# Optimization experiments

Hardware: AMD Instinct MI355X
Metric: run time of the kernel (lower is better)

## Reference

```python
import jax, jax.numpy as jnp
import numpy as np

D_MODEL = 1024
NUM_HEADS = 16
DEPTH = D_MODEL // NUM_HEADS
MAX_SEQ = 2048
B, S = 2, 2048


def setup_inputs() -> dict:
    key = jax.random.key(0)
    ks = jax.random.split(key, 12)
    scale = 1.0 / np.sqrt(D_MODEL)
    inp = {
        'q': jax.random.normal(ks[0], (B, S, D_MODEL), jnp.float32),
        'k': jax.random.normal(ks[1], (B, S, D_MODEL), jnp.float32),
        'v': jax.random.normal(ks[2], (B, S, D_MODEL), jnp.float32),
        'mask': jnp.zeros((B, 1, S, S), jnp.float32),
        'wq_w': jax.random.normal(ks[3], (D_MODEL, D_MODEL), jnp.float32) * scale,
        'wq_b': jnp.zeros((D_MODEL,), jnp.float32),
        'wk_w': jax.random.normal(ks[4], (D_MODEL, D_MODEL), jnp.float32) * scale,
        'wk_b': jnp.zeros((D_MODEL,), jnp.float32),
        'wv_w': jax.random.normal(ks[5], (D_MODEL, D_MODEL), jnp.float32) * scale,
        'wv_b': jnp.zeros((D_MODEL,), jnp.float32),
        'dense_w': jax.random.normal(ks[6], (D_MODEL, D_MODEL), jnp.float32) * scale,
        'dense_b': jnp.zeros((D_MODEL,), jnp.float32),
        'rel_bias': jax.random.normal(ks[7], (2 * MAX_SEQ - 1, NUM_HEADS), jnp.float32),
    }
    return inp


def _split_heads(x):
    # [B, S, D_MODEL] -> [B, H, S, depth]
    b, s, _ = x.shape
    return x.reshape(b, s, NUM_HEADS, DEPTH).transpose(0, 2, 1, 3)


def reference(q, k, v, mask, wq_w, wq_b, wk_w, wk_b, wv_w, wv_b, dense_w, dense_b, rel_bias):
    b, s, _ = q.shape
    # torch Linear: y = x @ W.T + b
    qh = _split_heads(q @ wq_w.T + wq_b)
    kh = _split_heads(k @ wk_w.T + wk_b)
    vh = _split_heads(v @ wv_w.T + wv_b)
    logits = jnp.einsum('bhqd,bhkd->bhqk', qh, kh) / jnp.sqrt(jnp.float32(DEPTH))
    # relative position bias gather
    pos = jnp.arange(s)
    idx = jnp.clip(pos[:, None] - pos[None, :] + MAX_SEQ - 1, 0, 2 * MAX_SEQ - 2)  # [S, S]
    pos_bias = rel_bias[idx]                      # [S, S, H]
    pos_bias = pos_bias.transpose(2, 0, 1)[None]  # [1, H, S, S]
    logits = logits + pos_bias + mask * (-1e9)
    attn = jax.nn.softmax(logits, axis=-1)        # dropout is identity in eval
    out = jnp.einsum('bhqk,bhkd->bhqd', attn, vh)
    out = out.transpose(0, 2, 1, 3).reshape(b, s, D_MODEL)
    out = out @ dense_w.T + dense_b
    return out, attn
```

## Files before the change

kernel.cpp:

```cpp
#include <hip/hip_runtime.h>

typedef _Float16 f16x8 __attribute__((ext_vector_type(8)));
typedef _Float16 f16x4 __attribute__((ext_vector_type(4)));
typedef float f32x4 __attribute__((ext_vector_type(4)));
typedef unsigned short u16x8 __attribute__((ext_vector_type(8)));
typedef unsigned int u32;

#define MFMA16H(a, b, c) __builtin_amdgcn_mfma_f32_16x16x32_f16(a, b, c, 0, 0, 0)

#if __has_builtin(__builtin_amdgcn_exp2f)
#define EXP2F(x) __builtin_amdgcn_exp2f(x)
#else
#define EXP2F(x) exp2f(x)
#endif

#define LOG2E 1.44269504088896340736f
#define SHIFT2 5.0f

__device__ __forceinline__ unsigned short f2bf(float x) {
  unsigned u = __float_as_uint(x);
  u += 0x7FFF + ((u >> 16) & 1);
  return (unsigned short)(u >> 16);
}
__device__ __forceinline__ float bf2f(unsigned short h) {
  return __uint_as_float(((unsigned)h) << 16);
}
__device__ __forceinline__ f16x8 ldh8(const _Float16* p) {
  return *reinterpret_cast<const f16x8*>(p);
}
__device__ __forceinline__ u16x8 ldu8(const unsigned short* p) {
  return *reinterpret_cast<const u16x8*>(p);
}
__device__ __forceinline__ f16x8 cvt8(float4 a, float4 b) {
  f16x8 r;
  r[0] = (_Float16)a.x; r[1] = (_Float16)a.y; r[2] = (_Float16)a.z; r[3] = (_Float16)a.w;
  r[4] = (_Float16)b.x; r[5] = (_Float16)b.y; r[6] = (_Float16)b.z; r[7] = (_Float16)b.w;
  return r;
}

__global__ __launch_bounds__(256) void prep_mask_perm(const float* __restrict__ src,
                                                      unsigned short* __restrict__ dst) {
  const int blk = blockIdx.x;
  const int kt = blk & 31, bq = blk >> 5;
  const int b = bq >> 5, qt = bq & 31;
  const int lane = threadIdx.x;
  const int w = lane >> 6, lg = (lane >> 4) & 3, lr = lane & 15;
  const int q0 = qt * 64;
  const float cs = -1e9f * LOG2E;
  unsigned short vals[16];
#pragma unroll
  for (int c = 0; c < 4; ++c)
#pragma unroll
    for (int r = 0; r < 4; ++r) {
      const int qr = q0 + w * 16 + lg * 4 + r;
      const int kc = kt * 64 + c * 16 + lr;
      vals[c * 4 + r] = f2bf(src[((size_t)b * 2048 + qr) * 2048 + kc] * cs);
    }
  uint4* out = reinterpret_cast<uint4*>(dst) + ((size_t)blk * 256 + lane) * 2;
  out[0] = *reinterpret_cast<uint4*>(&vals[0]);
  out[1] = *reinterpret_cast<uint4*>(&vals[8]);
}

__global__ __launch_bounds__(256, 3) void proj_gemm_kernel(
    const float* __restrict__ qin, const float* __restrict__ kin, const float* __restrict__ vin,
    const float* __restrict__ wq, const float* __restrict__ wk, const float* __restrict__ wv,
    const float* __restrict__ bq, const float* __restrict__ bk, const float* __restrict__ bv,
    _Float16* __restrict__ qhf, _Float16* __restrict__ khf, _Float16* __restrict__ vhT) {
  __shared__ __align__(16) _Float16 As[128 * 32];
  __shared__ __align__(16) _Float16 Bs[128 * 32];

  const int mode = blockIdx.x >> 8;
  const int t = blockIdx.x & 255;
  const float* A = mode == 0 ? qin : (mode == 1 ? kin : vin);
  const float* B = mode == 0 ? wq : (mode == 1 ? wk : wv);
  const float* bias = mode == 0 ? bq : (mode == 1 ? bk : bv);
  _Float16* outp = mode == 0 ? qhf : (mode == 1 ? khf : vhT);

  const int tid = threadIdx.x;
  const int tm = t & 31, tn = t >> 5;
  const int m0 = tm * 128, n0 = tn * 128;
  const int w = tid >> 6, l = tid & 63, lg = l >> 4, lr = l & 15;
  const int wr = w >> 1, wc = w & 1;
  const int srow = tid >> 2, scol = (tid & 3) * 8;

  f32x4 acc[4][4] = {};

  for (int kt = 0; kt < 32; ++kt) {
    const int k0 = kt * 32;
    float4 ra[2][2], rb[2][2];
#pragma unroll
    for (int it = 0; it < 2; ++it) {
      const int row = it * 64 + srow;
      const float* pa = A + (size_t)(m0 + row) * 1024 + k0 + scol;
      const float* pb = B + (size_t)(n0 + row) * 1024 + k0 + scol;
      ra[it][0] = *reinterpret_cast<const float4*>(pa);
      ra[it][1] = *reinterpret_cast<const float4*>(pa + 4);
      rb[it][0] = *reinterpret_cast<const float4*>(pb);
      rb[it][1] = *reinterpret_cast<const float4*>(pb + 4);
    }
    __syncthreads();
#pragma unroll
    for (int it = 0; it < 2; ++it) {
      const int eo = (it * 256 + tid) * 8;
      *reinterpret_cast<f16x8*>(As + eo) = cvt8(ra[it][0], ra[it][1]);
      *reinterpret_cast<f16x8*>(Bs + eo) = cvt8(rb[it][0], rb[it][1]);
    }
    __syncthreads();

    f16x8 fa[4], fb[4];
#pragma unroll
    for (int i = 0; i < 4; ++i) {
      fa[i] = ldh8(As + (wr * 64 + i * 16 + lr) * 32 + lg * 8);
      fb[i] = ldh8(Bs + (wc * 64 + i * 16 + lr) * 32 + lg * 8);
    }
#pragma unroll
    for (int i = 0; i < 4; ++i)
#pragma unroll
      for (int j = 0; j < 4; ++j)
        acc[i][j] = MFMA16H(fa[i], fb[j], acc[i][j]);
  }

#pragma unroll
  for (int i = 0; i < 4; ++i) {
    const int mrow = m0 + wr * 64 + i * 16 + lg * 4;
#pragma unroll
    for (int j = 0; j < 4; ++j) {
      const int ncol = n0 + wc * 64 + j * 16 + lr;
      const float bv = bias[ncol];
#pragma unroll
      for (int r = 0; r < 4; ++r) {
        const int m = mrow + r;
        const float v = acc[i][j][r] + bv;
        const int bb = m >> 11, s = m & 2047, hh = ncol >> 6, d = ncol & 63;
        if (mode != 2)
          outp[((size_t)(bb * 16 + hh) * 2048 + s) * 64 + d] = (_Float16)v;
        else
          outp[((size_t)(bb * 16 + hh) * 64 + d) * 2048 + s] = (_Float16)v;
      }
    }
  }
}

__global__ __launch_bounds__(256) void dense_gemm_kernel(
    const _Float16* __restrict__ A, const float* __restrict__ B,
    const float* __restrict__ bias, float* __restrict__ out_f) {
  __shared__ __align__(16) _Float16 As[128 * 32];
  __shared__ __align__(16) _Float16 Bs[128 * 32];

  const int tid = threadIdx.x;
  const int tm = blockIdx.x & 31, tn = blockIdx.x >> 5;
  const int m0 = tm * 128, n0 = tn * 128;
  const int w = tid >> 6, l = tid & 63, lg = l >> 4, lr = l & 15;
  const int wr = w >> 1, wc = w & 1;
  const int srow = tid >> 2, scol = (tid & 3) * 8;

  f32x4 acc[4][4] = {};

  for (int kt = 0; kt < 32; ++kt) {
    const int k0 = kt * 32;
    uint4 ra[2];
    float4 rb[2][2];
#pragma unroll
    for (int it = 0; it < 2; ++it) {
      const int row = it * 64 + srow;
      ra[it] = *reinterpret_cast<const uint4*>(A + (size_t)(m0 + row) * 1024 + k0 + scol);
      const float* pb = B + (size_t)(n0 + row) * 1024 + k0 + scol;
      rb[it][0] = *reinterpret_cast<const float4*>(pb);
      rb[it][1] = *reinterpret_cast<const float4*>(pb + 4);
    }
    __syncthreads();
#pragma unroll
    for (int it = 0; it < 2; ++it) {
      const int eo = (it * 256 + tid) * 8;
      *reinterpret_cast<uint4*>(As + eo) = ra[it];
      *reinterpret_cast<f16x8*>(Bs + eo) = cvt8(rb[it][0], rb[it][1]);
    }
    __syncthreads();

    f16x8 fa[4], fb[4];
#pragma unroll
    for (int i = 0; i < 4; ++i) {
      fa[i] = ldh8(As + (wr * 64 + i * 16 + lr) * 32 + lg * 8);
      fb[i] = ldh8(Bs + (wc * 64 + i * 16 + lr) * 32 + lg * 8);
    }
#pragma unroll
    for (int i = 0; i < 4; ++i)
#pragma unroll
      for (int j = 0; j < 4; ++j)
        acc[i][j] = MFMA16H(fa[i], fb[j], acc[i][j]);
  }

#pragma unroll
  for (int i = 0; i < 4; ++i) {
    const int mrow = m0 + wr * 64 + i * 16 + lg * 4;
#pragma unroll
    for (int j = 0; j < 4; ++j) {
      const int ncol = n0 + wc * 64 + j * 16 + lr;
      const float bv = bias[ncol];
#pragma unroll
      for (int r = 0; r < 4; ++r)
        out_f[(size_t)(mrow + r) * 1024 + ncol] = acc[i][j][r] + bv;
    }
  }
}

__global__ __launch_bounds__(256, 2) void attn_pv_kernel(
    const _Float16* __restrict__ qh, const _Float16* __restrict__ kh,
    const _Float16* __restrict__ vT,
    const float* __restrict__ rel_bias, const unsigned short* __restrict__ mperm,
    _Float16* __restrict__ o_h, _Float16* __restrict__ p16,
    float* __restrict__ scal) {
  __shared__ float rb2[2112];
  __shared__ __align__(16) _Float16 p_lds[64 * 76];

  const int bid = blockIdx.x;
  const int wg = ((bid & 7) << 7) | (bid >> 3);
  const int bh = wg >> 5, qt = wg & 31;
  const int b = bh >> 4, h = bh & 15;
  const int q0 = qt * 64;
  const int tid = threadIdx.x;
  const int w = tid >> 6, l = tid & 63, lg = l >> 4, lr = l & 15;

  for (int t = tid; t < 2111; t += 256)
    rb2[t] = rel_bias[(q0 + t) * 16 + h] * LOG2E - SHIFT2;

  const size_t bh_off = (size_t)bh * 2048 * 64;
  const _Float16* qhb = qh + bh_off;
  const _Float16* khb = kh + bh_off;
  const _Float16* vTb = vT + bh_off;
  const unsigned short* mpb =
      mperm + (((size_t)(b * 32 + qt) * 32) * 256 + tid) * 16;
  _Float16* pbh = p16 + (size_t)bh * 2048 * 2048;

  f16x8 qf[2];
  {
    const size_t qrow = (size_t)(q0 + w * 16 + lr) * 64;
    qf[0] = ldh8(qhb + qrow + lg * 8);
    qf[1] = ldh8(qhb + qrow + 32 + lg * 8);
  }
  __syncthreads();

  const int qbase = w * 16 + lg * 4;
  const float c1 = 0.125f * LOG2E;
  float sacc[4] = {0.f, 0.f, 0.f, 0.f};
  f32x4 acc_o[4] = {};

  f16x8 kA[8], kB[8];
  u16x8 mA[2], mB[2];

  auto loadK = [&](int kt, f16x8* kd, u16x8* md) {
    md[0] = ldu8(mpb + (size_t)kt * 4096);
    md[1] = ldu8(mpb + (size_t)kt * 4096 + 8);
#pragma unroll
    for (int c = 0; c < 4; ++c) {
      const _Float16* kr = khb + (size_t)(kt * 64 + c * 16 + lr) * 64 + lg * 8;
      kd[c * 2] = ldh8(kr);
      kd[c * 2 + 1] = ldh8(kr + 32);
    }
  };

  auto step = [&](int kt, const f16x8* kd, const u16x8* md) {
#pragma unroll
    for (int c = 0; c < 4; ++c) {
      f32x4 acc = {};
      acc = MFMA16H(qf[0], kd[c * 2], acc);
      acc = MFMA16H(qf[1], kd[c * 2 + 1], acc);
      const int kc = kt * 64 + c * 16 + lr;
#pragma unroll
      for (int r = 0; r < 4; ++r) {
        const float mbf = bf2f((unsigned short)md[c >> 1][(c & 1) * 4 + r]);
        const float l2 = fmaf(acc[r], c1, rb2[qbase + r - kc + 2047]) + mbf;
        const float p = EXP2F(l2);
        sacc[r] += p;
        p_lds[(qbase + r) * 76 + c * 16 + lr] = (_Float16)p;
      }
    }
    f16x8 pf0 = ldh8(p_lds + (w * 16 + lr) * 76 + lg * 8);
    f16x8 pf1 = ldh8(p_lds + (w * 16 + lr) * 76 + 32 + lg * 8);
    _Float16* prow = pbh + (size_t)(q0 + w * 16 + lr) * 2048 + kt * 64 + lg * 8;
    *reinterpret_cast<f16x8*>(prow) = pf0;
    *reinterpret_cast<f16x8*>(prow + 32) = pf1;
#pragma unroll
    for (int n = 0; n < 4; ++n) {
      const _Float16* vr = vTb + (size_t)(n * 16 + lr) * 2048 + kt * 64 + lg * 8;
      acc_o[n] = MFMA16H(pf0, ldh8(vr), acc_o[n]);
      acc_o[n] = MFMA16H(pf1, ldh8(vr + 32), acc_o[n]);
    }
  };

  loadK(0, kA, mA);
  for (int kt = 0; kt < 32; kt += 2) {
    loadK(kt + 1, kB, mB);
    step(kt, kA, mA);
    loadK((kt + 2) & 31, kA, mA);
    step(kt + 1, kB, mB);
  }

  float inv_s[4];
#pragma unroll
  for (int r = 0; r < 4; ++r) {
    float s = sacc[r];
    s += __shfl_xor(s, 1);
    s += __shfl_xor(s, 2);
    s += __shfl_xor(s, 4);
    s += __shfl_xor(s, 8);
    inv_s[r] = 1.0f / s;
    if (lr == 0) scal[(size_t)bh * 2048 + q0 + qbase + r] = inv_s[r];
  }

#pragma unroll
  for (int n = 0; n < 4; ++n)
#pragma unroll
    for (int r = 0; r < 4; ++r) {
      const int qr = q0 + qbase + r;
      const int d = n * 16 + lr;
      o_h[((size_t)(b * 2048 + qr) * 16 + h) * 64 + d] = (_Float16)(acc_o[n][r] * inv_s[r]);
    }
}

__global__ __launch_bounds__(256) void fixup_kernel(const _Float16* __restrict__ p16,
                                                    const float* __restrict__ scal,
                                                    float* __restrict__ attn) {
  const long long n8 = 16777216LL;
  const long long stride = (long long)gridDim.x * 256;
  for (long long i = (long long)blockIdx.x * 256 + threadIdx.x; i < n8; i += stride) {
    f16x8 p = reinterpret_cast<const f16x8*>(p16)[i];
    const float s = scal[i >> 8];
    float4 lo = make_float4((float)p[0] * s, (float)p[1] * s,
                            (float)p[2] * s, (float)p[3] * s);
    float4 hi = make_float4((float)p[4] * s, (float)p[5] * s,
                            (float)p[6] * s, (float)p[7] * s);
    reinterpret_cast<float4*>(attn)[2 * i] = lo;
    reinterpret_cast<float4*>(attn)[2 * i + 1] = hi;
  }
}

extern "C" void kernel_launch(void* const* d_in, const int* in_sizes, int n_in,
                              void* d_out, int out_size, void* d_ws, size_t ws_size,
                              hipStream_t stream) {
  const float* q = (const float*)d_in[0];
  const float* k = (const float*)d_in[1];
  const float* v = (const float*)d_in[2];
  const float* mask = (const float*)d_in[3];
  const float* wq_w = (const float*)d_in[4];
  const float* wq_b = (const float*)d_in[5];
  const float* wk_w = (const float*)d_in[6];
  const float* wk_b = (const float*)d_in[7];
  const float* wv_w = (const float*)d_in[8];
  const float* wv_b = (const float*)d_in[9];
  const float* dw = (const float*)d_in[10];
  const float* db = (const float*)d_in[11];
  const float* rel = (const float*)d_in[12];

  char* ws = (char*)d_ws;
  _Float16* qhf  = (_Float16*)(ws + 0);
  _Float16* khf  = (_Float16*)(ws + 8388608);
  _Float16* vhT  = (_Float16*)(ws + 16777216);
  _Float16* o_h  = (_Float16*)(ws + 25165824);
  float* scal    = (float*)(ws + 33554432);
  unsigned short* mperm = (unsigned short*)(ws + 33816576);
  _Float16* p16  = (_Float16*)(ws + 50593792);

  float* out = (float*)d_out;
  float* attn_out = out + 4194304;

  prep_mask_perm<<<2048, 256, 0, stream>>>(mask, mperm);

  proj_gemm_kernel<<<768, 256, 0, stream>>>(q, k, v, wq_w, wk_w, wv_w,
                                            wq_b, wk_b, wv_b, qhf, khf, vhT);

  attn_pv_kernel<<<1024, 256, 0, stream>>>(qhf, khf, vhT, rel, mperm, o_h, p16, scal);

  fixup_kernel<<<4096, 256, 0, stream>>>(p16, scal, attn_out);

  dense_gemm_kernel<<<256, 256, 0, stream>>>(o_h, dw, db, out);
}
```

Before: 611.8 us.

## Pre-convert inputs to fp16, merge kernels, and use nontemporal attn stores

A new prep kernel fuses the mask permutation with an fp32-to-fp16 conversion of q/k/v and all weight matrices, so the projection and dense GEMMs load fp16 directly instead of converting while staging. The dense GEMM and the attention fixup are merged into a single tail kernel launch, and the fixup writes attn with nontemporal stores. The attention kernel drops its double-buffered K/mask prefetch in favour of a simple loop and raises the occupancy hint to 4 blocks. The changes save launches and GEMM conversion work, but add an extra round trip of fp16 activations through memory and lose the explicit load prefetch in attention.

```diff
diff --git a/kernel.cpp b/kernel.cpp
--- a/kernel.cpp
+++ b/kernel.cpp
@@ -31,51 +31,61 @@
 __device__ __forceinline__ u16x8 ldu8(const unsigned short* p) {
   return *reinterpret_cast<const u16x8*>(p);
 }
-__device__ __forceinline__ f16x8 cvt8(float4 a, float4 b) {
-  f16x8 r;
-  r[0] = (_Float16)a.x; r[1] = (_Float16)a.y; r[2] = (_Float16)a.z; r[3] = (_Float16)a.w;
-  r[4] = (_Float16)b.x; r[5] = (_Float16)b.y; r[6] = (_Float16)b.z; r[7] = (_Float16)b.w;
-  return r;
-}
-
-__global__ __launch_bounds__(256) void prep_mask_perm(const float* __restrict__ src,
-                                                      unsigned short* __restrict__ dst) {
-  const int blk = blockIdx.x;
-  const int kt = blk & 31, bq = blk >> 5;
-  const int b = bq >> 5, qt = bq & 31;
-  const int lane = threadIdx.x;
-  const int w = lane >> 6, lg = (lane >> 4) & 3, lr = lane & 15;
-  const int q0 = qt * 64;
-  const float cs = -1e9f * LOG2E;
-  unsigned short vals[16];
-#pragma unroll
-  for (int c = 0; c < 4; ++c)
-#pragma unroll
-    for (int r = 0; r < 4; ++r) {
-      const int qr = q0 + w * 16 + lg * 4 + r;
-      const int kc = kt * 64 + c * 16 + lr;
-      vals[c * 4 + r] = f2bf(src[((size_t)b * 2048 + qr) * 2048 + kc] * cs);
-    }
-  uint4* out = reinterpret_cast<uint4*>(dst) + ((size_t)blk * 256 + lane) * 2;
-  out[0] = *reinterpret_cast<uint4*>(&vals[0]);
-  out[1] = *reinterpret_cast<uint4*>(&vals[8]);
-}
-
-__global__ __launch_bounds__(256, 3) void proj_gemm_kernel(
-    const float* __restrict__ qin, const float* __restrict__ kin, const float* __restrict__ vin,
+
+__global__ __launch_bounds__(256) void prep_kernel(
+    const float* __restrict__ q, const float* __restrict__ k, const float* __restrict__ v,
     const float* __restrict__ wq, const float* __restrict__ wk, const float* __restrict__ wv,
-    const float* __restrict__ bq, const float* __restrict__ bk, const float* __restrict__ bv,
-    _Float16* __restrict__ qhf, _Float16* __restrict__ khf, _Float16* __restrict__ vhT) {
-  __shared__ __align__(16) _Float16 As[128 * 32];
-  __shared__ __align__(16) _Float16 Bs[128 * 32];
-
-  const int mode = blockIdx.x >> 8;
-  const int t = blockIdx.x & 255;
-  const float* A = mode == 0 ? qin : (mode == 1 ? kin : vin);
-  const float* B = mode == 0 ? wq : (mode == 1 ? wk : wv);
-  const float* bias = mode == 0 ? bq : (mode == 1 ? bk : bv);
-  _Float16* outp = mode == 0 ? qhf : (mode == 1 ? khf : vhT);
-
+    const float* __restrict__ dwt, const float* __restrict__ mask,
+    _Float16* __restrict__ qf, _Float16* __restrict__ kf, _Float16* __restrict__ vf,
+    _Float16* __restrict__ wqf, _Float16* __restrict__ wkf, _Float16* __restrict__ wvf,
+    _Float16* __restrict__ dwf, unsigned short* __restrict__ mperm) {
+  if (blockIdx.x < 2048) {
+    const int blk = blockIdx.x;
+    const int kt = blk & 31, bq = blk >> 5;
+    const int b = bq >> 5, qt = bq & 31;
+    const int lane = threadIdx.x;
+    const int w = lane >> 6, lg = (lane >> 4) & 3, lr = lane & 15;
+    const int q0 = qt * 64;
+    const float cs = -1e9f * LOG2E;
+    unsigned short vals[16];
+#pragma unroll
+    for (int c = 0; c < 4; ++c)
+#pragma unroll
+      for (int r = 0; r < 4; ++r) {
+        const int qr = q0 + w * 16 + lg * 4 + r;
+        const int kc = kt * 64 + c * 16 + lr;
+        vals[c * 4 + r] = f2bf(mask[((size_t)b * 2048 + qr) * 2048 + kc] * cs);
+      }
+    uint4* out = reinterpret_cast<uint4*>(mperm) + ((size_t)blk * 256 + lane) * 2;
+    out[0] = *reinterpret_cast<uint4*>(&vals[0]);
+    out[1] = *reinterpret_cast<uint4*>(&vals[8]);
+    return;
+  }
+  const int i = (blockIdx.x - 2048) * 256 + threadIdx.x;
+  const int r = i >> 18;
+  const int j = i & 262143;
+  const float* src;
+  _Float16* dst;
+  int off = 0;
+  if (r < 4)       { src = q;   dst = qf;  off = r * 262144; }
+  else if (r < 8)  { src = k;   dst = kf;  off = (r - 4) * 262144; }
+  else if (r < 12) { src = v;   dst = vf;  off = (r - 8) * 262144; }
+  else if (r == 12){ src = wq;  dst = wqf; }
+  else if (r == 13){ src = wk;  dst = wkf; }
+  else if (r == 14){ src = wv;  dst = wvf; }
+  else             { src = dwt; dst = dwf; }
+  const int g = off + j;
+  float4 x = reinterpret_cast<const float4*>(src)[g];
+  f16x4 h;
+  h[0] = (_Float16)x.x; h[1] = (_Float16)x.y;
+  h[2] = (_Float16)x.z; h[3] = (_Float16)x.w;
+  reinterpret_cast<f16x4*>(dst)[g] = h;
+}
+
+__device__ __forceinline__ void gemm_body(
+    int t, int mode, const _Float16* __restrict__ A, const _Float16* __restrict__ B,
+    const float* __restrict__ bias, _Float16* __restrict__ out_h, float* __restrict__ out_f,
+    _Float16* As, _Float16* Bs) {
   const int tid = threadIdx.x;
   const int tm = t & 31, tn = t >> 5;
   const int m0 = tm * 128, n0 = tn * 128;
@@ -87,23 +97,19 @@
 
   for (int kt = 0; kt < 32; ++kt) {
     const int k0 = kt * 32;
-    float4 ra[2][2], rb[2][2];
+    uint4 ra[2], rb[2];
 #pragma unroll
     for (int it = 0; it < 2; ++it) {
       const int row = it * 64 + srow;
-      const float* pa = A + (size_t)(m0 + row) * 1024 + k0 + scol;
-      const float* pb = B + (size_t)(n0 + row) * 1024 + k0 + scol;
-      ra[it][0] = *reinterpret_cast<const float4*>(pa);
-      ra[it][1] = *reinterpret_cast<const float4*>(pa + 4);
-      rb[it][0] = *reinterpret_cast<const float4*>(pb);
-      rb[it][1] = *reinterpret_cast<const float4*>(pb + 4);
+      ra[it] = *reinterpret_cast<const uint4*>(A + (size_t)(m0 + row) * 1024 + k0 + scol);
+      rb[it] = *reinterpret_cast<const uint4*>(B + (size_t)(n0 + row) * 1024 + k0 + scol);
     }
     __syncthreads();
 #pragma unroll
     for (int it = 0; it < 2; ++it) {
       const int eo = (it * 256 + tid) * 8;
-      *reinterpret_cast<f16x8*>(As + eo) = cvt8(ra[it][0], ra[it][1]);
-      *reinterpret_cast<f16x8*>(Bs + eo) = cvt8(rb[it][0], rb[it][1]);
+      *reinterpret_cast<uint4*>(As + eo) = ra[it];
+      *reinterpret_cast<uint4*>(Bs + eo) = rb[it];
     }
     __syncthreads();
 
@@ -131,80 +137,35 @@
       for (int r = 0; r < 4; ++r) {
         const int m = mrow + r;
         const float v = acc[i][j][r] + bv;
-        const int bb = m >> 11, s = m & 2047, hh = ncol >> 6, d = ncol & 63;
-        if (mode != 2)
-          outp[((size_t)(bb * 16 + hh) * 2048 + s) * 64 + d] = (_Float16)v;
-        else
-          outp[((size_t)(bb * 16 + hh) * 64 + d) * 2048 + s] = (_Float16)v;
+        if (mode == 2) {
+          out_f[(size_t)m * 1024 + ncol] = v;
+        } else {
+          const int bb = m >> 11, s = m & 2047, hh = ncol >> 6, d = ncol & 63;
+          if (mode == 0)
+            out_h[((size_t)(bb * 16 + hh) * 2048 + s) * 64 + d] = (_Float16)v;
+          else
+            out_h[((size_t)(bb * 16 + hh) * 64 + d) * 2048 + s] = (_Float16)v;
+        }
       }
     }
   }
 }
 
-__global__ __launch_bounds__(256) void dense_gemm_kernel(
-    const _Float16* __restrict__ A, const float* __restrict__ B,
-    const float* __restrict__ bias, float* __restrict__ out_f) {
+__global__ __launch_bounds__(256, 3) void proj_gemm_kernel(
+    const _Float16* __restrict__ qf, const _Float16* __restrict__ kf, const _Float16* __restrict__ vf,
+    const _Float16* __restrict__ wqf, const _Float16* __restrict__ wkf, const _Float16* __restrict__ wvf,
+    const float* __restrict__ bq, const float* __restrict__ bk, const float* __restrict__ bv,
+    _Float16* __restrict__ qhf, _Float16* __restrict__ khf, _Float16* __restrict__ vhT) {
   __shared__ __align__(16) _Float16 As[128 * 32];
   __shared__ __align__(16) _Float16 Bs[128 * 32];
-
-  const int tid = threadIdx.x;
-  const int tm = blockIdx.x & 31, tn = blockIdx.x >> 5;
-  const int m0 = tm * 128, n0 = tn * 128;
-  const int w = tid >> 6, l = tid & 63, lg = l >> 4, lr = l & 15;
-  const int wr = w >> 1, wc = w & 1;
-  const int srow = tid >> 2, scol = (tid & 3) * 8;
-
-  f32x4 acc[4][4] = {};
-
-  for (int kt = 0; kt < 32; ++kt) {
-    const int k0 = kt * 32;
-    uint4 ra[2];
-    float4 rb[2][2];
-#pragma unroll
-    for (int it = 0; it < 2; ++it) {
-      const int row = it * 64 + srow;
-      ra[it] = *reinterpret_cast<const uint4*>(A + (size_t)(m0 + row) * 1024 + k0 + scol);
-      const float* pb = B + (size_t)(n0 + row) * 1024 + k0 + scol;
-      rb[it][0] = *reinterpret_cast<const float4*>(pb);
-      rb[it][1] = *reinterpret_cast<const float4*>(pb + 4);
-    }
-    __syncthreads();
-#pragma unroll
-    for (int it = 0; it < 2; ++it) {
-      const int eo = (it * 256 + tid) * 8;
-      *reinterpret_cast<uint4*>(As + eo) = ra[it];
-      *reinterpret_cast<f16x8*>(Bs + eo) = cvt8(rb[it][0], rb[it][1]);
-    }
-    __syncthreads();
-
-    f16x8 fa[4], fb[4];
-#pragma unroll
-    for (int i = 0; i < 4; ++i) {
-      fa[i] = ldh8(As + (wr * 64 + i * 16 + lr) * 32 + lg * 8);
-      fb[i] = ldh8(Bs + (wc * 64 + i * 16 + lr) * 32 + lg * 8);
-    }
-#pragma unroll
-    for (int i = 0; i < 4; ++i)
-#pragma unroll
-      for (int j = 0; j < 4; ++j)
-        acc[i][j] = MFMA16H(fa[i], fb[j], acc[i][j]);
-  }
-
-#pragma unroll
-  for (int i = 0; i < 4; ++i) {
-    const int mrow = m0 + wr * 64 + i * 16 + lg * 4;
-#pragma unroll
-    for (int j = 0; j < 4; ++j) {
-      const int ncol = n0 + wc * 64 + j * 16 + lr;
-      const float bv = bias[ncol];
-#pragma unroll
-      for (int r = 0; r < 4; ++r)
-        out_f[(size_t)(mrow + r) * 1024 + ncol] = acc[i][j][r] + bv;
-    }
-  }
-}
-
-__global__ __launch_bounds__(256, 2) void attn_pv_kernel(
+  const int mode = blockIdx.x >> 8;
+  const int t = blockIdx.x & 255;
+  if (mode == 0)      gemm_body(t, 0, qf, wqf, bq, qhf, nullptr, As, Bs);
+  else if (mode == 1) gemm_body(t, 0, kf, wkf, bk, khf, nullptr, As, Bs);
+  else                gemm_body(t, 1, vf, wvf, bv, vhT, nullptr, As, Bs);
+}
+
+__global__ __launch_bounds__(256, 4) void attn_pv_kernel(
     const _Float16* __restrict__ qh, const _Float16* __restrict__ kh,
     const _Float16* __restrict__ vT,
     const float* __restrict__ rel_bias, const unsigned short* __restrict__ mperm,
@@ -245,30 +206,20 @@
   float sacc[4] = {0.f, 0.f, 0.f, 0.f};
   f32x4 acc_o[4] = {};
 
-  f16x8 kA[8], kB[8];
-  u16x8 mA[2], mB[2];
-
-  auto loadK = [&](int kt, f16x8* kd, u16x8* md) {
-    md[0] = ldu8(mpb + (size_t)kt * 4096);
-    md[1] = ldu8(mpb + (size_t)kt * 4096 + 8);
+  for (int kt = 0; kt < 32; ++kt) {
+    u16x8 m0v = ldu8(mpb + (size_t)kt * 4096);
+    u16x8 m1v = ldu8(mpb + (size_t)kt * 4096 + 8);
 #pragma unroll
     for (int c = 0; c < 4; ++c) {
-      const _Float16* kr = khb + (size_t)(kt * 64 + c * 16 + lr) * 64 + lg * 8;
-      kd[c * 2] = ldh8(kr);
-      kd[c * 2 + 1] = ldh8(kr + 32);
-    }
-  };
-
-  auto step = [&](int kt, const f16x8* kd, const u16x8* md) {
-#pragma unroll
-    for (int c = 0; c < 4; ++c) {
+      const int kc = kt * 64 + c * 16 + lr;
+      const _Float16* kr = khb + (size_t)kc * 64 + lg * 8;
       f32x4 acc = {};
-      acc = MFMA16H(qf[0], kd[c * 2], acc);
-      acc = MFMA16H(qf[1], kd[c * 2 + 1], acc);
-      const int kc = kt * 64 + c * 16 + lr;
+      acc = MFMA16H(qf[0], ldh8(kr), acc);
+      acc = MFMA16H(qf[1], ldh8(kr + 32), acc);
 #pragma unroll
       for (int r = 0; r < 4; ++r) {
-        const float mbf = bf2f((unsigned short)md[c >> 1][(c & 1) * 4 + r]);
+        const float mbf = bf2f((c < 2) ? (unsigned short)m0v[(c & 1) * 4 + r]
+                                       : (unsigned short)m1v[(c & 1) * 4 + r]);
         const float l2 = fmaf(acc[r], c1, rb2[qbase + r - kc + 2047]) + mbf;
         const float p = EXP2F(l2);
         sacc[r] += p;
@@ -286,14 +237,6 @@
       acc_o[n] = MFMA16H(pf0, ldh8(vr), acc_o[n]);
       acc_o[n] = MFMA16H(pf1, ldh8(vr + 32), acc_o[n]);
     }
-  };
-
-  loadK(0, kA, mA);
-  for (int kt = 0; kt < 32; kt += 2) {
-    loadK(kt + 1, kB, mB);
-    step(kt, kA, mA);
-    loadK((kt + 2) & 31, kA, mA);
-    step(kt + 1, kB, mB);
   }
 
   float inv_s[4];
@@ -318,20 +261,30 @@
     }
 }
 
-__global__ __launch_bounds__(256) void fixup_kernel(const _Float16* __restrict__ p16,
-                                                    const float* __restrict__ scal,
-                                                    float* __restrict__ attn) {
+__global__ __launch_bounds__(256) void tail_kernel(
+    const _Float16* __restrict__ A, const _Float16* __restrict__ Bw,
+    const float* __restrict__ bias, float* __restrict__ out_f,
+    const _Float16* __restrict__ p16, const float* __restrict__ scal,
+    float* __restrict__ attn) {
+  __shared__ __align__(16) _Float16 As[128 * 32];
+  __shared__ __align__(16) _Float16 Bs[128 * 32];
+  if (blockIdx.x < 256) {
+    gemm_body(blockIdx.x, 2, A, Bw, bias, nullptr, out_f, As, Bs);
+    return;
+  }
+  f32x4* attnv = reinterpret_cast<f32x4*>(attn);
   const long long n8 = 16777216LL;
-  const long long stride = (long long)gridDim.x * 256;
-  for (long long i = (long long)blockIdx.x * 256 + threadIdx.x; i < n8; i += stride) {
+  const long long stride = (long long)(gridDim.x - 256) * 256;
+  for (long long i = (long long)(blockIdx.x - 256) * 256 + threadIdx.x; i < n8; i += stride) {
     f16x8 p = reinterpret_cast<const f16x8*>(p16)[i];
     const float s = scal[i >> 8];
-    float4 lo = make_float4((float)p[0] * s, (float)p[1] * s,
-                            (float)p[2] * s, (float)p[3] * s);
-    float4 hi = make_float4((float)p[4] * s, (float)p[5] * s,
-                            (float)p[6] * s, (float)p[7] * s);
-    reinterpret_cast<float4*>(attn)[2 * i] = lo;
-    reinterpret_cast<float4*>(attn)[2 * i + 1] = hi;
+    f32x4 lo, hi;
+    lo[0] = (float)p[0] * s; lo[1] = (float)p[1] * s;
+    lo[2] = (float)p[2] * s; lo[3] = (float)p[3] * s;
+    hi[0] = (float)p[4] * s; hi[1] = (float)p[5] * s;
+    hi[2] = (float)p[6] * s; hi[3] = (float)p[7] * s;
+    __builtin_nontemporal_store(lo, attnv + 2 * i);
+    __builtin_nontemporal_store(hi, attnv + 2 * i + 1);
   }
 }
 
@@ -353,25 +306,31 @@
   const float* rel = (const float*)d_in[12];
 
   char* ws = (char*)d_ws;
-  _Float16* qhf  = (_Float16*)(ws + 0);
-  _Float16* khf  = (_Float16*)(ws + 8388608);
-  _Float16* vhT  = (_Float16*)(ws + 16777216);
-  _Float16* o_h  = (_Float16*)(ws + 25165824);
-  float* scal    = (float*)(ws + 33554432);
-  unsigned short* mperm = (unsigned short*)(ws + 33816576);
-  _Float16* p16  = (_Float16*)(ws + 50593792);
+  _Float16* qf_in = (_Float16*)(ws + 0);
+  _Float16* kf_in = (_Float16*)(ws + 8388608);
+  _Float16* vf_in = (_Float16*)(ws + 16777216);
+  _Float16* wqf   = (_Float16*)(ws + 25165824);
+  _Float16* wkf   = (_Float16*)(ws + 27262976);
+  _Float16* wvf   = (_Float16*)(ws + 29360128);
+  _Float16* dwf   = (_Float16*)(ws + 31457280);
+  _Float16* qhf   = (_Float16*)(ws + 33554432);
+  _Float16* khf   = (_Float16*)(ws + 41943040);
+  _Float16* vhT   = (_Float16*)(ws + 50331648);
+  _Float16* o_h   = (_Float16*)(ws + 58720256);
+  float* scal     = (float*)(ws + 67108864);
+  unsigned short* mperm = (unsigned short*)(ws + 67371008);
+  _Float16* p16   = (_Float16*)(ws + 84148224);
 
   float* out = (float*)d_out;
   float* attn_out = out + 4194304;
 
-  prep_mask_perm<<<2048, 256, 0, stream>>>(mask, mperm);
-
-  proj_gemm_kernel<<<768, 256, 0, stream>>>(q, k, v, wq_w, wk_w, wv_w,
+  prep_kernel<<<18432, 256, 0, stream>>>(q, k, v, wq_w, wk_w, wv_w, dw, mask,
+                                         qf_in, kf_in, vf_in, wqf, wkf, wvf, dwf, mperm);
+
+  proj_gemm_kernel<<<768, 256, 0, stream>>>(qf_in, kf_in, vf_in, wqf, wkf, wvf,
                                             wq_b, wk_b, wv_b, qhf, khf, vhT);
 
   attn_pv_kernel<<<1024, 256, 0, stream>>>(qhf, khf, vhT, rel, mperm, o_h, p16, scal);
 
-  fixup_kernel<<<4096, 256, 0, stream>>>(p16, scal, attn_out);
-
-  dense_gemm_kernel<<<256, 256, 0, stream>>>(o_h, dw, db, out);
-}
+  tail_kernel<<<2304, 256, 0, stream>>>(o_h, dwf, db, out, p16, scal, attn_out);
+}
```

Result: slower. 626.6 us (+2.4%).
